# Kernel tuning notes

Hardware: AMD Instinct MI355X
Metric: run time of the kernel (lower is better)

The kernel has to match this reference:

```python
import jax, jax.numpy as jnp
from jax import lax
import numpy as np

KERNEL_SIZE = 15
CHANNELS = 3
PAD = KERNEL_SIZE // 2


def _make_kernels(sigma):
    """Gaussian kernels [B, K, K], normalized to sum 1 (matches torch create_kernel)."""
    k = KERNEL_SIZE
    ax = jnp.linspace(-(k - 1) / 2.0, (k - 1) / 2.0, k, dtype=sigma.dtype)
    xx, yy = jnp.meshgrid(ax, ax, indexing='ij')  # [K, K]
    s = sigma.reshape(-1, 1, 1)  # [B, 1, 1]
    kern = jnp.exp(-(xx[None] ** 2 + yy[None] ** 2) / (2.0 * s ** 2 + 1e-8))
    kern = kern / (kern.sum(axis=(-1, -2), keepdims=True) + 1e-8)
    return kern  # [B, K, K]


def setup_inputs() -> dict:
    key = jax.random.key(0)
    k1, k2 = jax.random.split(key)
    x = jax.random.normal(k1, (32, CHANNELS, 512, 512), dtype=jnp.float32)
    # sigma in (0.5, 3.0): realistic blur stddevs, strictly positive
    sigma = jax.random.uniform(k2, (32,), dtype=jnp.float32, minval=0.5, maxval=3.0)
    return {"x": x, "sigma": sigma}


def reference(x, sigma):
    B, C, H, W = x.shape
    kern = _make_kernels(sigma)  # [B, K, K]

    def conv_one(xi, ki):
        # xi: [C, H, W], ki: [K, K]; same kernel replicated per channel (depthwise)
        w = jnp.broadcast_to(ki[None, None], (C, 1, KERNEL_SIZE, KERNEL_SIZE))
        out = lax.conv_general_dilated(
            xi[None],  # [1, C, H, W]
            w,         # [C, 1, K, K]
            window_strides=(1, 1),
            padding=[(PAD, PAD), (PAD, PAD)],
            feature_group_count=C,
        )
        return out[0]  # [C, H, W]

    return jax.vmap(conv_one)(x, kern)  # [B, C, H, W]
```

## Files before the change

### kernel.cpp

```cpp
#include <hip/hip_runtime.h>

#define CHANNELS 3
#define HW 512
#define KS 15
#define GPAD 7
#define TILE_W 64
#define TILE_H 32
#define HT (TILE_H + 2 * GPAD)
#define IN_STR 81
#define WCOLS 20
#define NSTAGE (HT * WCOLS)
#define WIN (16 + KS - 1)

__global__ __launch_bounds__(256, 8)
void gauss_blur_kernel(const float* __restrict__ x,
                       const float* __restrict__ sigma,
                       float* __restrict__ out) {
    __shared__ float in_s[HT * IN_STR];

    const int tid   = threadIdx.x;
    const int tileX = blockIdx.x;
    const int tileY = blockIdx.y;
    const int bc    = blockIdx.z;
    const int b     = bc / CHANNELS;

    const size_t plane = (size_t)HW * HW;
    const float* xp = x + (size_t)bc * plane;
    float* op       = out + (size_t)bc * plane;
    const int gx0 = tileX * TILE_W;
    const int gy0 = tileY * TILE_H - GPAD;
    const int ax0 = gx0 - 8;

    float4 v[4];
    int   rr[4], qq[4];
    bool  ok[4];
    #pragma unroll
    for (int s = 0; s < 4; ++s) {
        const int i = tid + 256 * s;
        ok[s] = (i < NSTAGE);
        const int r = i / WCOLS;
        const int q = i - r * WCOLS;
        rr[s] = r; qq[s] = q;
        v[s] = make_float4(0.f, 0.f, 0.f, 0.f);
        if (ok[s]) {
            const int gy = gy0 + r;
            const int gc = ax0 + 4 * q;
            if ((unsigned)gy < (unsigned)HW) {
                const float* rowp = xp + (size_t)gy * HW;
                if (gc >= 0 && gc + 4 <= HW) {
                    v[s] = *(const float4*)(rowp + gc);
                } else {
                    if ((unsigned)(gc + 0) < (unsigned)HW) v[s].x = rowp[gc + 0];
                    if ((unsigned)(gc + 1) < (unsigned)HW) v[s].y = rowp[gc + 1];
                    if ((unsigned)(gc + 2) < (unsigned)HW) v[s].z = rowp[gc + 2];
                    if ((unsigned)(gc + 3) < (unsigned)HW) v[s].w = rowp[gc + 3];
                }
            }
        }
    }

    float w[KS];
    {
        const float s = sigma[b];
        const float inv_denom = 1.0f / (2.0f * s * s + 1e-8f);
        float g[KS];
        float sum = 0.0f;
        #pragma unroll
        for (int i = 0; i < KS; ++i) {
            const float d = (float)(i - GPAD);
            g[i] = __expf(-d * d * inv_denom);
            sum += g[i];
        }
        const float inv = 1.0f / sum;
        #pragma unroll
        for (int i = 0; i < KS; ++i)
            w[i] = __int_as_float(__builtin_amdgcn_readfirstlane(__float_as_int(g[i] * inv)));
    }

    #pragma unroll
    for (int s = 0; s < 4; ++s) {
        if (ok[s]) {
            float* d = &in_s[rr[s] * IN_STR + 4 * qq[s]];
            d[0] = v[s].x; d[1] = v[s].y; d[2] = v[s].z; d[3] = v[s].w;
        }
    }
    __syncthreads();

    float acc[16];
    #pragma unroll
    for (int o = 0; o < 16; ++o) acc[o] = 0.0f;
    const bool hwork = (tid < HT * 4);
    if (hwork) {
        const int r  = tid >> 2;
        const int ch = tid & 3;
        const float* src = &in_s[r * IN_STR + 16 * ch + 1];
        #pragma unroll
        for (int j = 0; j < WIN; ++j) {
            const float vv = src[j];
            const int lo = (j - (KS - 1)) > 0 ? (j - (KS - 1)) : 0;
            const int hi = (j < 15) ? j : 15;
            #pragma unroll
            for (int o = lo; o <= hi; ++o)
                acc[o] = fmaf(w[j - o], vv, acc[o]);
        }
    }
    __syncthreads();

    if (hwork) {
        const int r  = tid >> 2;
        const int ch = tid & 3;
        float* dst = &in_s[r * IN_STR + 16 * ch];
        #pragma unroll
        for (int o = 0; o < 16; ++o) dst[o] = acc[o];
    }
    __syncthreads();

    {
        const int c  = tid & (TILE_W - 1);
        const int r0 = (tid >> 6) * 8;
        float vacc[8];
        #pragma unroll
        for (int o = 0; o < 8; ++o) vacc[o] = 0.0f;
        #pragma unroll
        for (int j = 0; j < 8 + KS - 1; ++j) {
            const float vv = in_s[(r0 + j) * IN_STR + c];
            const int lo = (j - (KS - 1)) > 0 ? (j - (KS - 1)) : 0;
            const int hi = (j < 8) ? j : 7;
            #pragma unroll
            for (int o = lo; o <= hi; ++o)
                vacc[o] = fmaf(w[j - o], vv, vacc[o]);
        }
        float* colp = op + (size_t)(tileY * TILE_H + r0) * HW + gx0 + c;
        #pragma unroll
        for (int o = 0; o < 8; ++o)
            colp[(size_t)o * HW] = vacc[o];
    }
}

extern "C" void kernel_launch(void* const* d_in, const int* in_sizes, int n_in,
                              void* d_out, int out_size, void* d_ws, size_t ws_size,
                              hipStream_t stream) {
    const float* x     = (const float*)d_in[0];
    const float* sigma = (const float*)d_in[1];
    float* out         = (float*)d_out;
    const int B = in_sizes[1];
    dim3 grid(HW / TILE_W, HW / TILE_H, B * CHANNELS);
    gauss_blur_kernel<<<grid, dim3(256, 1, 1), 0, stream>>>(x, sigma, out);
}
```

Measured before the change: 178.9 us.

## Reshape tile to 32x64 and add fast unchecked load path for interior tiles

Changes the output tile from 64 wide by 32 tall to 32 wide by 64 tall, with matching shared-memory stride, staging column count and thread mapping for the horizontal and vertical passes. This lowers the redundant horizontal-pass work spent on the vertical halo rows. It also adds a branch-free float4 load path for tiles that cannot touch the image border, and recomputes staging indices instead of holding them in registers. The cost is a wider relative horizontal halo to load and shorter 32-float store rows per wavefront half.

Result: no change. 182.1 us (+1.8%).

```diff
diff --git a/kernel.cpp b/kernel.cpp
--- a/kernel.cpp
+++ b/kernel.cpp
@@ -4,12 +4,13 @@
 #define HW 512
 #define KS 15
 #define GPAD 7
-#define TILE_W 64
-#define TILE_H 32
+#define TILE_W 32
+#define TILE_H 64
 #define HT (TILE_H + 2 * GPAD)
-#define IN_STR 81
-#define WCOLS 20
+#define IN_STR 49
+#define WCOLS 12
 #define NSTAGE (HT * WCOLS)
+#define NH (HT * (TILE_W / 16))
 #define WIN (16 + KS - 1)
 
 __global__ __launch_bounds__(256, 8)
@@ -30,30 +31,41 @@
     const int gx0 = tileX * TILE_W;
     const int gy0 = tileY * TILE_H - GPAD;
     const int ax0 = gx0 - 8;
+    const bool interior = (tileX >= 1) && (tileX <= (HW / TILE_W) - 2) &&
+                          (tileY >= 1) && (tileY <= (HW / TILE_H) - 2);
 
     float4 v[4];
-    int   rr[4], qq[4];
-    bool  ok[4];
     #pragma unroll
-    for (int s = 0; s < 4; ++s) {
-        const int i = tid + 256 * s;
-        ok[s] = (i < NSTAGE);
-        const int r = i / WCOLS;
-        const int q = i - r * WCOLS;
-        rr[s] = r; qq[s] = q;
-        v[s] = make_float4(0.f, 0.f, 0.f, 0.f);
-        if (ok[s]) {
-            const int gy = gy0 + r;
-            const int gc = ax0 + 4 * q;
-            if ((unsigned)gy < (unsigned)HW) {
-                const float* rowp = xp + (size_t)gy * HW;
-                if (gc >= 0 && gc + 4 <= HW) {
-                    v[s] = *(const float4*)(rowp + gc);
-                } else {
-                    if ((unsigned)(gc + 0) < (unsigned)HW) v[s].x = rowp[gc + 0];
-                    if ((unsigned)(gc + 1) < (unsigned)HW) v[s].y = rowp[gc + 1];
-                    if ((unsigned)(gc + 2) < (unsigned)HW) v[s].z = rowp[gc + 2];
-                    if ((unsigned)(gc + 3) < (unsigned)HW) v[s].w = rowp[gc + 3];
+    for (int s = 0; s < 4; ++s) v[s] = make_float4(0.f, 0.f, 0.f, 0.f);
+    if (interior) {
+        #pragma unroll
+        for (int s = 0; s < 4; ++s) {
+            const int i = tid + 256 * s;
+            if (i < NSTAGE) {
+                const int r = i / WCOLS;
+                const int q = i - r * WCOLS;
+                v[s] = *(const float4*)(xp + (size_t)(gy0 + r) * HW + (ax0 + 4 * q));
+            }
+        }
+    } else {
+        #pragma unroll
+        for (int s = 0; s < 4; ++s) {
+            const int i = tid + 256 * s;
+            if (i < NSTAGE) {
+                const int r  = i / WCOLS;
+                const int q  = i - r * WCOLS;
+                const int gy = gy0 + r;
+                const int gc = ax0 + 4 * q;
+                if ((unsigned)gy < (unsigned)HW) {
+                    const float* rowp = xp + (size_t)gy * HW;
+                    if (gc >= 0 && gc + 4 <= HW) {
+                        v[s] = *(const float4*)(rowp + gc);
+                    } else {
+                        if ((unsigned)(gc + 0) < (unsigned)HW) v[s].x = rowp[gc + 0];
+                        if ((unsigned)(gc + 1) < (unsigned)HW) v[s].y = rowp[gc + 1];
+                        if ((unsigned)(gc + 2) < (unsigned)HW) v[s].z = rowp[gc + 2];
+                        if ((unsigned)(gc + 3) < (unsigned)HW) v[s].w = rowp[gc + 3];
+                    }
                 }
             }
         }
@@ -79,8 +91,11 @@
 
     #pragma unroll
     for (int s = 0; s < 4; ++s) {
-        if (ok[s]) {
-            float* d = &in_s[rr[s] * IN_STR + 4 * qq[s]];
+        const int i = tid + 256 * s;
+        if (i < NSTAGE) {
+            const int r = i / WCOLS;
+            const int q = i - r * WCOLS;
+            float* d = &in_s[r * IN_STR + 4 * q];
             d[0] = v[s].x; d[1] = v[s].y; d[2] = v[s].z; d[3] = v[s].w;
         }
     }
@@ -89,10 +104,10 @@
     float acc[16];
     #pragma unroll
     for (int o = 0; o < 16; ++o) acc[o] = 0.0f;
-    const bool hwork = (tid < HT * 4);
+    const bool hwork = (tid < NH);
     if (hwork) {
-        const int r  = tid >> 2;
-        const int ch = tid & 3;
+        const int r  = tid >> 1;
+        const int ch = tid & 1;
         const float* src = &in_s[r * IN_STR + 16 * ch + 1];
         #pragma unroll
         for (int j = 0; j < WIN; ++j) {
@@ -107,8 +122,8 @@
     __syncthreads();
 
     if (hwork) {
-        const int r  = tid >> 2;
-        const int ch = tid & 3;
+        const int r  = tid >> 1;
+        const int ch = tid & 1;
         float* dst = &in_s[r * IN_STR + 16 * ch];
         #pragma unroll
         for (int o = 0; o < 16; ++o) dst[o] = acc[o];
@@ -117,7 +132,7 @@
 
     {
         const int c  = tid & (TILE_W - 1);
-        const int r0 = (tid >> 6) * 8;
+        const int r0 = (tid >> 5) * 8;
         float vacc[8];
         #pragma unroll
         for (int o = 0; o < 8; ++o) vacc[o] = 0.0f;
```

## Process several planes per block with register-prefetched next-plane loads

Applied to the files above, without the earlier changes.

Each block now loops over six batch-channel planes of the same tile. While the current plane is being convolved, the global loads for the next plane are issued into registers. Interior tiles also take a fast path that skips bounds checks, and offsets are precomputed once per block. The aim is to hide global memory latency and amortise setup cost, at the price of more registers, an extra barrier per plane and a grid that is six times smaller.

After: 229.1 us. 28.0% more time.

```diff
diff --git a/kernel.cpp b/kernel.cpp
--- a/kernel.cpp
+++ b/kernel.cpp
@@ -10,130 +10,155 @@
 #define IN_STR 81
 #define WCOLS 20
 #define NSTAGE (HT * WCOLS)
+#define NH (HT * 4)
 #define WIN (16 + KS - 1)
+#define NZB 6
 
 __global__ __launch_bounds__(256, 8)
 void gauss_blur_kernel(const float* __restrict__ x,
                        const float* __restrict__ sigma,
-                       float* __restrict__ out) {
+                       float* __restrict__ out, const int BC) {
     __shared__ float in_s[HT * IN_STR];
 
     const int tid   = threadIdx.x;
     const int tileX = blockIdx.x;
     const int tileY = blockIdx.y;
-    const int bc    = blockIdx.z;
-    const int b     = bc / CHANNELS;
+    const int z0    = blockIdx.z * NZB;
 
     const size_t plane = (size_t)HW * HW;
-    const float* xp = x + (size_t)bc * plane;
-    float* op       = out + (size_t)bc * plane;
     const int gx0 = tileX * TILE_W;
     const int gy0 = tileY * TILE_H - GPAD;
     const int ax0 = gx0 - 8;
+    const bool interior = (tileX >= 1) && (tileX <= (HW / TILE_W) - 2) &&
+                          (tileY >= 1) && (tileY <= (HW / TILE_H) - 2);
 
-    float4 v[4];
-    int   rr[4], qq[4];
-    bool  ok[4];
+    int  ldsoff[4], goff[4], grow[4], gcol[4];
+    bool ok[4];
     #pragma unroll
     for (int s = 0; s < 4; ++s) {
         const int i = tid + 256 * s;
         ok[s] = (i < NSTAGE);
         const int r = i / WCOLS;
         const int q = i - r * WCOLS;
-        rr[s] = r; qq[s] = q;
-        v[s] = make_float4(0.f, 0.f, 0.f, 0.f);
-        if (ok[s]) {
-            const int gy = gy0 + r;
-            const int gc = ax0 + 4 * q;
-            if ((unsigned)gy < (unsigned)HW) {
-                const float* rowp = xp + (size_t)gy * HW;
-                if (gc >= 0 && gc + 4 <= HW) {
-                    v[s] = *(const float4*)(rowp + gc);
-                } else {
-                    if ((unsigned)(gc + 0) < (unsigned)HW) v[s].x = rowp[gc + 0];
-                    if ((unsigned)(gc + 1) < (unsigned)HW) v[s].y = rowp[gc + 1];
-                    if ((unsigned)(gc + 2) < (unsigned)HW) v[s].z = rowp[gc + 2];
-                    if ((unsigned)(gc + 3) < (unsigned)HW) v[s].w = rowp[gc + 3];
+        ldsoff[s] = r * IN_STR + 4 * q;
+        grow[s] = gy0 + r;
+        gcol[s] = ax0 + 4 * q;
+        goff[s] = grow[s] * HW + gcol[s];
+    }
+    const int vc   = tid & (TILE_W - 1);
+    const int vr0  = (tid >> 6) * 8;
+    const int voff = (tileY * TILE_H + vr0) * HW + gx0 + vc;
+
+    float4 v[4];
+    auto issue_loads = [&](const float* xp) {
+        if (interior) {
+            #pragma unroll
+            for (int s = 0; s < 4; ++s)
+                if (ok[s]) v[s] = *(const float4*)(xp + goff[s]);
+        } else {
+            #pragma unroll
+            for (int s = 0; s < 4; ++s) {
+                v[s] = make_float4(0.f, 0.f, 0.f, 0.f);
+                if (ok[s] && (unsigned)grow[s] < (unsigned)HW) {
+                    const float* rowp = xp + (size_t)grow[s] * HW;
+                    const int gc = gcol[s];
+                    if (gc >= 0 && gc + 4 <= HW) {
+                        v[s] = *(const float4*)(rowp + gc);
+                    } else {
+                        if ((unsigned)(gc + 0) < (unsigned)HW) v[s].x = rowp[gc + 0];
+                        if ((unsigned)(gc + 1) < (unsigned)HW) v[s].y = rowp[gc + 1];
+                        if ((unsigned)(gc + 2) < (unsigned)HW) v[s].z = rowp[gc + 2];
+                        if ((unsigned)(gc + 3) < (unsigned)HW) v[s].w = rowp[gc + 3];
+                    }
                 }
             }
         }
-    }
+    };
 
-    float w[KS];
-    {
-        const float s = sigma[b];
-        const float inv_denom = 1.0f / (2.0f * s * s + 1e-8f);
-        float g[KS];
-        float sum = 0.0f;
+    issue_loads(x + (size_t)z0 * plane);
+
+    for (int t = 0; t < NZB; ++t) {
+        const int bc = z0 + t;
+        if (bc >= BC) break;
+
+        float w[KS];
+        {
+            const float s = sigma[bc / CHANNELS];
+            const float inv_denom = 1.0f / (2.0f * s * s + 1e-8f);
+            float g[KS];
+            float sum = 0.0f;
+            #pragma unroll
+            for (int i = 0; i < KS; ++i) {
+                const float d = (float)(i - GPAD);
+                g[i] = __expf(-d * d * inv_denom);
+                sum += g[i];
+            }
+            const float inv = 1.0f / sum;
+            #pragma unroll
+            for (int i = 0; i < KS; ++i)
+                w[i] = __int_as_float(__builtin_amdgcn_readfirstlane(__float_as_int(g[i] * inv)));
+        }
+
+        __syncthreads();
+
         #pragma unroll
-        for (int i = 0; i < KS; ++i) {
-            const float d = (float)(i - GPAD);
-            g[i] = __expf(-d * d * inv_denom);
-            sum += g[i];
+        for (int s = 0; s < 4; ++s) {
+            if (ok[s]) {
+                float* d = &in_s[ldsoff[s]];
+                d[0] = v[s].x; d[1] = v[s].y; d[2] = v[s].z; d[3] = v[s].w;
+            }
         }
-        const float inv = 1.0f / sum;
+        if (t + 1 < NZB && bc + 1 < BC)
+            issue_loads(x + (size_t)(bc + 1) * plane);
+        __syncthreads();
+
+        float acc[16];
         #pragma unroll
-        for (int i = 0; i < KS; ++i)
-            w[i] = __int_as_float(__builtin_amdgcn_readfirstlane(__float_as_int(g[i] * inv)));
-    }
+        for (int o = 0; o < 16; ++o) acc[o] = 0.0f;
+        const bool hwork = (tid < NH);
+        if (hwork) {
+            const int r  = tid >> 2;
+            const int ch = tid & 3;
+            const float* src = &in_s[r * IN_STR + 16 * ch + 1];
+            #pragma unroll
+            for (int j = 0; j < WIN; ++j) {
+                const float vv = src[j];
+                const int lo = (j - (KS - 1)) > 0 ? (j - (KS - 1)) : 0;
+                const int hi = (j < 15) ? j : 15;
+                #pragma unroll
+                for (int o = lo; o <= hi; ++o)
+                    acc[o] = fmaf(w[j - o], vv, acc[o]);
+            }
+        }
+        __syncthreads();
 
-    #pragma unroll
-    for (int s = 0; s < 4; ++s) {
-        if (ok[s]) {
-            float* d = &in_s[rr[s] * IN_STR + 4 * qq[s]];
-            d[0] = v[s].x; d[1] = v[s].y; d[2] = v[s].z; d[3] = v[s].w;
+        if (hwork) {
+            const int r  = tid >> 2;
+            const int ch = tid & 3;
+            float* dst = &in_s[r * IN_STR + 16 * ch];
+            #pragma unroll
+            for (int o = 0; o < 16; ++o) dst[o] = acc[o];
         }
-    }
-    __syncthreads();
+        __syncthreads();
 
-    float acc[16];
-    #pragma unroll
-    for (int o = 0; o < 16; ++o) acc[o] = 0.0f;
-    const bool hwork = (tid < HT * 4);
-    if (hwork) {
-        const int r  = tid >> 2;
-        const int ch = tid & 3;
-        const float* src = &in_s[r * IN_STR + 16 * ch + 1];
-        #pragma unroll
-        for (int j = 0; j < WIN; ++j) {
-            const float vv = src[j];
-            const int lo = (j - (KS - 1)) > 0 ? (j - (KS - 1)) : 0;
-            const int hi = (j < 15) ? j : 15;
+        {
+            float vacc[8];
             #pragma unroll
-            for (int o = lo; o <= hi; ++o)
-                acc[o] = fmaf(w[j - o], vv, acc[o]);
+            for (int o = 0; o < 8; ++o) vacc[o] = 0.0f;
+            #pragma unroll
+            for (int j = 0; j < 8 + KS - 1; ++j) {
+                const float vv = in_s[(vr0 + j) * IN_STR + vc];
+                const int lo = (j - (KS - 1)) > 0 ? (j - (KS - 1)) : 0;
+                const int hi = (j < 8) ? j : 7;
+                #pragma unroll
+                for (int o = lo; o <= hi; ++o)
+                    vacc[o] = fmaf(w[j - o], vv, vacc[o]);
+            }
+            float* colp = out + (size_t)bc * plane + voff;
+            #pragma unroll
+            for (int o = 0; o < 8; ++o)
+                colp[(size_t)o * HW] = vacc[o];
         }
-    }
-    __syncthreads();
-
-    if (hwork) {
-        const int r  = tid >> 2;
-        const int ch = tid & 3;
-        float* dst = &in_s[r * IN_STR + 16 * ch];
-        #pragma unroll
-        for (int o = 0; o < 16; ++o) dst[o] = acc[o];
-    }
-    __syncthreads();
-
-    {
-        const int c  = tid & (TILE_W - 1);
-        const int r0 = (tid >> 6) * 8;
-        float vacc[8];
-        #pragma unroll
-        for (int o = 0; o < 8; ++o) vacc[o] = 0.0f;
-        #pragma unroll
-        for (int j = 0; j < 8 + KS - 1; ++j) {
-            const float vv = in_s[(r0 + j) * IN_STR + c];
-            const int lo = (j - (KS - 1)) > 0 ? (j - (KS - 1)) : 0;
-            const int hi = (j < 8) ? j : 7;
-            #pragma unroll
-            for (int o = lo; o <= hi; ++o)
-                vacc[o] = fmaf(w[j - o], vv, vacc[o]);
-        }
-        float* colp = op + (size_t)(tileY * TILE_H + r0) * HW + gx0 + c;
-        #pragma unroll
-        for (int o = 0; o < 8; ++o)
-            colp[(size_t)o * HW] = vacc[o];
     }
 }
 
@@ -143,7 +168,8 @@
     const float* x     = (const float*)d_in[0];
     const float* sigma = (const float*)d_in[1];
     float* out         = (float*)d_out;
-    const int B = in_sizes[1];
-    dim3 grid(HW / TILE_W, HW / TILE_H, B * CHANNELS);
-    gauss_blur_kernel<<<grid, dim3(256, 1, 1), 0, stream>>>(x, sigma, out);
+    const int B  = in_sizes[1];
+    const int BC = B * CHANNELS;
+    dim3 grid(HW / TILE_W, HW / TILE_H, (BC + NZB - 1) / NZB);
+    gauss_blur_kernel<<<grid, dim3(256, 1, 1), 0, stream>>>(x, sigma, out, BC);
 }
```
